# Optimization experiments

Measured on AMD Instinct MI355X. Metric: run time of the kernel, lower is better.

Reference implementation:

```python
import jax, jax.numpy as jnp
import numpy as np

N = 100000   # rows of edge_attr == number of graph nodes == number of edges (E == N required by index_add_)
B = 64       # number of graphs
IN_CH, HID, OUT_CH, FC_HID = 128, 128, 128, 256


def setup_inputs() -> dict:
    key = jax.random.key(0)
    ks = jax.random.split(key, 20)
    s = 0.05
    inp = {
        "edge_attr": jax.random.normal(ks[0], (N, 6, 120), dtype=jnp.float32),
        "edge_index": jax.random.randint(ks[1], (2, N), 0, N),
        "batch": jnp.sort(jax.random.randint(ks[2], (N,), 0, B)),
        "num_graphs": B,
        # Conv1d: in=6 -> 16 -> 32, k=5, pad=2
        "conv1_w": jax.random.normal(ks[3], (16, 6, 5), dtype=jnp.float32) * s,
        "conv1_b": jnp.zeros((16,), jnp.float32),
        "conv2_w": jax.random.normal(ks[4], (32, 16, 5), dtype=jnp.float32) * s,
        "conv2_b": jnp.zeros((32,), jnp.float32),
        # fc: 32*120 -> in_channels
        "fc_w": jax.random.normal(ks[5], (IN_CH, 32 * 120), dtype=jnp.float32) * s,
        "fc_b": jnp.zeros((IN_CH,), jnp.float32),
        # GCNConv layers (weight as [out, in], like torch Linear)
        "gcn1_w": jax.random.normal(ks[6], (HID, IN_CH), dtype=jnp.float32) * s,
        "gcn1_b": jnp.zeros((HID,), jnp.float32),
        "gcn2_w": jax.random.normal(ks[7], (OUT_CH, HID), dtype=jnp.float32) * s,
        "gcn2_b": jnp.zeros((OUT_CH,), jnp.float32),
        # MLP head
        "fc1_w": jax.random.normal(ks[8], (FC_HID, OUT_CH), dtype=jnp.float32) * s,
        "fc1_b": jnp.zeros((FC_HID,), jnp.float32),
        "fc2_w": jax.random.normal(ks[9], (OUT_CH, FC_HID), dtype=jnp.float32) * s,
        "fc2_b": jnp.zeros((OUT_CH,), jnp.float32),
    }
    return inp


def conv1d(x, w, b):
    # x: [N, C_in, L], w: [C_out, C_in, K], padding=2 (same)
    y = jax.lax.conv_general_dilated(
        x, w, window_strides=(1,), padding=[(2, 2)],
        dimension_numbers=("NCH", "OIH", "NCH"))
    return y + b[None, :, None]


def gcn_conv(x, edge_index, w, b, n_nodes):
    # PyG GCNConv: add self-loops, symmetric normalization deg^-1/2 A_hat deg^-1/2
    src, dst = edge_index[0], edge_index[1]
    loop = jnp.arange(n_nodes)
    src_f = jnp.concatenate([src, loop])
    dst_f = jnp.concatenate([dst, loop])
    deg = jax.ops.segment_sum(jnp.ones_like(src_f, dtype=x.dtype), dst_f,
                              num_segments=n_nodes)
    dinv = jnp.where(deg > 0, jax.lax.rsqrt(deg), 0.0)
    norm = dinv[src_f] * dinv[dst_f]                      # [E+N]
    h = x @ w.T                                           # [N, out]
    msg = h[src_f] * norm[:, None]                        # gather + scale
    return jax.ops.segment_sum(msg, dst_f, num_segments=n_nodes) + b


def reference(edge_attr, edge_index, batch, num_graphs,
              conv1_w, conv1_b, conv2_w, conv2_b, fc_w, fc_b,
              gcn1_w, gcn1_b, gcn2_w, gcn2_b,
              fc1_w, fc1_b, fc2_w, fc2_b):
    n = edge_attr.shape[0]
    x = jax.nn.relu(conv1d(edge_attr, conv1_w, conv1_b))   # [N,16,120]
    x = jax.nn.relu(conv1d(x, conv2_w, conv2_b))           # [N,32,120]
    x = x.reshape(n, -1)                                   # [N,3840]
    x = x @ fc_w.T + fc_b                                  # [N,in_channels]
    x = jax.nn.relu(gcn_conv(x, edge_index, gcn1_w, gcn1_b, n))
    x = gcn_conv(x, edge_index, gcn2_w, gcn2_b, n)         # [N,out_channels]
    # edge-to-batch scatter-add pooling: out[batch[row][e]] += x[e]
    row = edge_index[0]
    out = jax.ops.segment_sum(x, batch[row], num_segments=num_graphs)  # [B,out]
    x = jax.nn.relu(out @ fc1_w.T + fc1_b)
    x = x @ fc2_w.T + fc2_b
    return x
```

## Files before the change

kernel.cpp:

```cpp
#include <hip/hip_runtime.h>

typedef unsigned int u32;
typedef unsigned short u16;
typedef short short8 __attribute__((ext_vector_type(8)));
typedef float floatx4 __attribute__((ext_vector_type(4)));

static __device__ __forceinline__ u32 f2bf(float f) {
  u32 u = __float_as_uint(f);
  return (u + 0x7fffu + ((u >> 16) & 1u)) >> 16;
}
static __device__ __forceinline__ u32 cvtpk(float lo, float hi) {
  u32 r;
  asm("v_cvt_pk_bf16_f32 %0, %1, %2" : "=v"(r) : "v"(lo), "v"(hi));
  return r;
}


#define X0_ROWS 136
#define X1W_ROWS 66
#define X1W_LDA 24

__global__ __launch_bounds__(256, 2) void k_convfc(
    const float* __restrict__ ea,
    const u32* __restrict__ w1sw, const float* __restrict__ b1,
    const u32* __restrict__ w2sw, const float* __restrict__ b2,
    const u32* __restrict__ fcwsw, const float* __restrict__ fcb,
    float* __restrict__ xfc, int n, int ntiles)
{
  __shared__ __align__(16) u16 sX0[16][X0_ROWS * 8];
  __shared__ __align__(16) u16 sX1[4][X1W_ROWS * X1W_LDA];
  __shared__ __align__(16) u16 sF[32 * 64 * 8];

  const int t = threadIdx.x, lane = t & 63, wv = t >> 6;
  const int quad = lane >> 4, lr = lane & 15;

  for (int i = t; i < 16 * X0_ROWS * 4; i += 256) ((u32*)sX0)[i] = 0;

  short8 w1f[2], w2f[2][3];
#pragma unroll
  for (int kb = 0; kb < 2; ++kb) w1f[kb] = ((const short8*)w1sw)[kb * 64 + lane];
#pragma unroll
  for (int ot = 0; ot < 2; ++ot)
#pragma unroll
    for (int kb = 0; kb < 3; ++kb)
      w2f[ot][kb] = ((const short8*)w2sw)[(ot * 3 + kb) * 64 + lane];

  float b1r[4];
#pragma unroll
  for (int r = 0; r < 4; ++r) b1r[r] = b1[quad * 4 + r];
  const float bv20 = b2[lr], bv21 = b2[16 + lr];

  const int c0 = wv * 16 + lr, c1 = (wv + 4) * 16 + lr;
  const float bv0 = fcb[c0], bv1 = fcb[c1];
  const short8* bw = (const short8*)fcwsw;
  const short8* b0p = bw + ((size_t)wv * 128) * 64 + lane;
  const short8* b1p = bw + ((size_t)(wv + 4) * 128) * 64 + lane;
  const int j2base = wv * 4;

  __syncthreads();

  for (int tile = blockIdx.x; tile < ntiles; tile += gridDim.x) {
    const long node0 = (long)tile * 16;

#pragma unroll
    for (int it = 0; it < 8; ++it) {
      int idx = t + it * 256;
      int nd = idx >> 7, p = idx & 127;
      if (p < 120) {
        long gn = node0 + nd;
        float v0 = 0.f, v1 = 0.f, v2 = 0.f, v3 = 0.f, v4 = 0.f, v5 = 0.f;
        if (gn < n) {
          const float* base = ea + (size_t)gn * 720 + p;
          v0 = base[0];   v1 = base[120]; v2 = base[240];
          v3 = base[360]; v4 = base[480]; v5 = base[600];
        }
        u32 w0 = cvtpk(v0, v1), w1 = cvtpk(v2, v3), w2 = cvtpk(v4, v5);
        *(uint4*)&sX0[nd][(p + 2) * 8] = make_uint4(w0, w1, w2, 0u);
      }
    }
    __syncthreads();

    floatx4 acc0 = {bv0, bv0, bv0, bv0};
    floatx4 acc1 = {bv1, bv1, bv1, bv1};

#pragma unroll
    for (int r = 0; r < 4; ++r) {
      u16* x1 = sX1[wv];
      if (r == 0) {
        if (lane < 24) ((u32*)(x1 + 16 * X1W_LDA))[lane] = 0;
      } else if (r == 3) {
        u32* z = (u32*)(x1 + 42 * X1W_LDA);
#pragma unroll
        for (int i2 = 0; i2 < 3; ++i2) {
          int i = lane + i2 * 64;
          if (i < 132) z[i] = 0;
        }
      }
#pragma unroll 1
      for (int jj = 0; jj < 4; ++jj) {
        const int j2 = j2base + jj;
        const u16* x0n = sX0[j2];
#pragma unroll
        for (int q4 = 0; q4 < 4; ++q4) {
          const int ptp = 2 * r - 1 + q4;
          if (ptp >= 0 && ptp <= 7) {
            const int row0 = ptp * 16 + lr;
            short8 bx0 = *(const short8*)&x0n[(row0 + quad) * 8];
            short8 bx1 = *(const short8*)&x0n[(row0 + 4 + quad) * 8];
            floatx4 a1 = {b1r[0], b1r[1], b1r[2], b1r[3]};
            a1 = __builtin_amdgcn_mfma_f32_16x16x32_bf16(w1f[0], bx0, a1, 0, 0, 0);
            a1 = __builtin_amdgcn_mfma_f32_16x16x32_bf16(w1f[1], bx1, a1, 0, 0, 0);
            if (ptp < 7 || lr < 8) {
              const int lrow = row0 + 18 - 32 * r;
              u32 lo = cvtpk(fmaxf(a1[0], 0.0f), fmaxf(a1[1], 0.0f));
              u32 hi = cvtpk(fmaxf(a1[2], 0.0f), fmaxf(a1[3], 0.0f));
              *(uint2*)&x1[lrow * X1W_LDA + quad * 4] = make_uint2(lo, hi);
            }
          }
        }
        const int tq = quad >> 1, cq = (quad & 1) * 8;
#pragma unroll
        for (int ptl = 0; ptl < 2; ++ptl) {
          const int lrow0 = ptl * 16 + lr + 16;
          short8 ax0 = *(const short8*)&x1[(lrow0 + tq) * X1W_LDA + cq];
          short8 ax1 = *(const short8*)&x1[(lrow0 + 2 + tq) * X1W_LDA + cq];
          short8 ax2 = *(const short8*)&x1[(lrow0 + 4 + tq) * X1W_LDA + cq];
#pragma unroll
          for (int ot = 0; ot < 2; ++ot) {
            const float bb = ot ? bv21 : bv20;
            floatx4 a2 = {bb, bb, bb, bb};
            a2 = __builtin_amdgcn_mfma_f32_16x16x32_bf16(ax0, w2f[ot][0], a2, 0, 0, 0);
            a2 = __builtin_amdgcn_mfma_f32_16x16x32_bf16(ax1, w2f[ot][1], a2, 0, 0, 0);
            a2 = __builtin_amdgcn_mfma_f32_16x16x32_bf16(ax2, w2f[ot][2], a2, 0, 0, 0);
            u32 lo = cvtpk(fmaxf(a2[0], 0.0f), fmaxf(a2[1], 0.0f));
            u32 hi = cvtpk(fmaxf(a2[2], 0.0f), fmaxf(a2[3], 0.0f));
            const int o = ot * 16 + lr;
            const int s = (ptl * 2 + tq) * 16 + j2;
            const int G = o * 64 + (s ^ (o & 7));
            *(uint2*)&sF[G * 8 + (quad & 1) * 4] = make_uint2(lo, hi);
          }
        }
      }
      __syncthreads();

#pragma unroll 8
      for (int o = 0; o < 32; ++o) {
        short8 a = *(const short8*)&sF[(o * 64 + (lane ^ (o & 7))) * 8];
        const int ks = o * 4 + r;
        short8 bb0 = b0p[(size_t)ks * 64];
        short8 bb1 = b1p[(size_t)ks * 64];
        acc0 = __builtin_amdgcn_mfma_f32_16x16x32_bf16(a, bb0, acc0, 0, 0, 0);
        acc1 = __builtin_amdgcn_mfma_f32_16x16x32_bf16(a, bb1, acc1, 0, 0, 0);
      }
      __syncthreads();
    }

#pragma unroll
    for (int rr = 0; rr < 4; ++rr) {
      long node = node0 + quad * 4 + rr;
      if (node < n) {
        xfc[node * 128 + c0] = acc0[rr];
        xfc[node * 128 + c1] = acc1[rr];
      }
    }
  }
}

__global__ void k_prep(const float* __restrict__ fcw, const float* __restrict__ g1w,
                       const float* __restrict__ g2w, const float* __restrict__ w1,
                       const float* __restrict__ w2,
                       uint4* __restrict__ fcwsw, uint4* __restrict__ g1wsw,
                       uint4* __restrict__ g2wsw, uint4* __restrict__ w1sw,
                       uint4* __restrict__ w2sw,
                       float* __restrict__ dinv, float* __restrict__ pooled, int n)
{
  int gid = blockIdx.x * 256 + threadIdx.x;
  if (gid < 65536) {
    int e = gid, lane = e & 63, t2 = e >> 6, ks = t2 & 127, nt = t2 >> 7;
    int col = nt * 16 + (lane & 15);
    int k0 = ks * 32 + ((lane >> 4) & 3) * 8;
    u32 pk[4];
#pragma unroll
    for (int h = 0; h < 4; ++h) {
      u32 v01[2];
#pragma unroll
      for (int g = 0; g < 2; ++g) {
        int k = k0 + h * 2 + g;
        int o = k >> 7, p = k & 127;
        float v = (p < 120) ? fcw[(size_t)col * 3840 + o * 120 + p] : 0.0f;
        v01[g] = f2bf(v);
      }
      pk[h] = v01[0] | (v01[1] << 16);
    }
    fcwsw[e] = make_uint4(pk[0], pk[1], pk[2], pk[3]);
    return;
  }
  gid -= 65536;
  if (gid < 4096) {
    const float* gw = (gid < 2048) ? g1w : g2w;
    uint4* out = (gid < 2048) ? g1wsw : g2wsw;
    int e = gid & 2047, lane = e & 63;
    int col = (e >> 8) * 16 + (lane & 15);
    int k0 = ((e >> 6) & 3) * 32 + ((lane >> 4) & 3) * 8;
    u32 pk[4];
#pragma unroll
    for (int h = 0; h < 4; ++h)
      pk[h] = f2bf(gw[(size_t)col * 128 + k0 + h * 2]) |
              (f2bf(gw[(size_t)col * 128 + k0 + h * 2 + 1]) << 16);
    out[e] = make_uint4(pk[0], pk[1], pk[2], pk[3]);
    return;
  }
  gid -= 4096;
  if (gid < 128) {
    int e = gid, lane = e & 63, kb = e >> 6, cout = lane & 15;
    int k0 = kb * 32 + ((lane >> 4) & 3) * 8;
    u32 pk[4];
#pragma unroll
    for (int h = 0; h < 4; ++h) {
      u32 v01[2];
#pragma unroll
      for (int g = 0; g < 2; ++g) {
        int k = k0 + h * 2 + g, tap = k >> 3, cin = k & 7;
        float v = (tap < 5 && cin < 6) ? w1[cout * 30 + cin * 5 + tap] : 0.0f;
        v01[g] = f2bf(v);
      }
      pk[h] = v01[0] | (v01[1] << 16);
    }
    w1sw[e] = make_uint4(pk[0], pk[1], pk[2], pk[3]);
    return;
  }
  gid -= 128;
  if (gid < 384) {
    int e = gid, lane = e & 63, t2 = e >> 6;
    int kb = t2 % 3, ot = t2 / 3;
    int o = ot * 16 + (lane & 15);
    int k0 = kb * 32 + ((lane >> 4) & 3) * 8;
    u32 pk[4];
#pragma unroll
    for (int h = 0; h < 4; ++h) {
      u32 v01[2];
#pragma unroll
      for (int g = 0; g < 2; ++g) {
        int k = k0 + h * 2 + g, tap = k >> 4, c = k & 15;
        float v = (tap < 5) ? w2[o * 80 + c * 5 + tap] : 0.0f;
        v01[g] = f2bf(v);
      }
      pk[h] = v01[0] | (v01[1] << 16);
    }
    w2sw[e] = make_uint4(pk[0], pk[1], pk[2], pk[3]);
    return;
  }
  gid -= 384;
  if (gid < n) { dinv[gid] = 1.0f; return; }
  gid -= n;
  if (gid < 8192) pooled[gid] = 0.0f;
}

__global__ __launch_bounds__(256) void k_gcn_gemm(
    const float* __restrict__ X, const u32* __restrict__ wsw,
    const float* __restrict__ bias, const float* __restrict__ dinv,
    float* __restrict__ H, float* __restrict__ Out, int n, int relu)
{
  __shared__ __align__(16) u16 sA[16 * 136];
  __shared__ float sDi[16];
  const int t = threadIdx.x;
  const long node0 = (long)blockIdx.x * 16;
  {
    int nd = t >> 4, k0 = (t & 15) * 8;
    long node = node0 + nd;
    float v[8];
    if (node < n) {
      float4 f0 = *(const float4*)&X[node * 128 + k0];
      float4 f1 = *(const float4*)&X[node * 128 + k0 + 4];
      v[0]=f0.x; v[1]=f0.y; v[2]=f0.z; v[3]=f0.w; v[4]=f1.x; v[5]=f1.y; v[6]=f1.z; v[7]=f1.w;
      if (relu) {
#pragma unroll
        for (int i = 0; i < 8; ++i) v[i] = fmaxf(v[i], 0.0f);
      }
    } else {
#pragma unroll
      for (int i = 0; i < 8; ++i) v[i] = 0.0f;
    }
    u32 pk[4];
#pragma unroll
    for (int h = 0; h < 4; ++h) pk[h] = cvtpk(v[2*h], v[2*h+1]);
    *(uint4*)&sA[nd * 136 + k0] = make_uint4(pk[0], pk[1], pk[2], pk[3]);
    if (t < 16) sDi[t] = (node0 + t < n) ? dinv[node0 + t] : 0.0f;
  }
  __syncthreads();
  const int lane = t & 63, wv = t >> 6, quad = lane >> 4, lr = lane & 15;
  short8 af[4];
#pragma unroll
  for (int kb = 0; kb < 4; ++kb)
    af[kb] = *(const short8*)&sA[lr * 136 + kb * 32 + quad * 8];
#pragma unroll
  for (int h = 0; h < 2; ++h) {
    const int nt = wv + h * 4;
    const short8* bp = ((const short8*)wsw) + (nt * 4) * 64 + lane;
    floatx4 acc = {0.0f, 0.0f, 0.0f, 0.0f};
#pragma unroll
    for (int kb = 0; kb < 4; ++kb)
      acc = __builtin_amdgcn_mfma_f32_16x16x32_bf16(af[kb], bp[kb * 64], acc, 0, 0, 0);
    const int col = nt * 16 + lr;
    const float bcol = bias[col];
#pragma unroll
    for (int r = 0; r < 4; ++r) {
      long node = node0 + quad * 4 + r;
      if (node < n) {
        float hv = acc[r];
        float di = sDi[quad * 4 + r];
        H[node * 128 + col] = hv;
        Out[node * 128 + col] = bcol + di * di * hv;
      }
    }
  }
}

__global__ void k_scatter(const float* __restrict__ Hs, float* __restrict__ Out,
                          const int* __restrict__ src, const int* __restrict__ dst,
                          const float* __restrict__ dinv, int n)
{
  const int gid = blockIdx.x * blockDim.x + threadIdx.x;
  const int e = gid >> 6;
  const int lane = gid & 63;
  if (e >= n) return;
  const int s = src[e], d = dst[e];
  const float nrm = dinv[s] * dinv[d];
  const float2 v = *(const float2*)(Hs + (size_t)s * 128 + lane * 2);
  float* o = Out + (size_t)d * 128 + lane * 2;
  unsafeAtomicAdd(o, v.x * nrm);
  unsafeAtomicAdd(o + 1, v.y * nrm);
}

__global__ void k_deg(float* dinv, const int* __restrict__ dst, int n) {
  int i = blockIdx.x * 256 + threadIdx.x; if (i < n) unsafeAtomicAdd(&dinv[dst[i]], 1.0f);
}
__global__ void k_rsqrt(float* p, int n) {
  int i = blockIdx.x * 256 + threadIdx.x; if (i < n) p[i] = rsqrtf(p[i]);
}

__global__ __launch_bounds__(256) void k_pool(const float* __restrict__ X,
    const int* __restrict__ src, const int* __restrict__ batch,
    float* __restrict__ pooled, int n)
{
  __shared__ float sAcc[64 * 128];
  for (int i = threadIdx.x; i < 8192; i += 256) sAcc[i] = 0.0f;
  __syncthreads();
  const int c = threadIdx.x & 127, half = threadIdx.x >> 7;
  for (int e = blockIdx.x * 2 + half; e < n; e += gridDim.x * 2) {
    int g = batch[src[e]];
    atomicAdd(&sAcc[g * 128 + c], X[(size_t)e * 128 + c]);
  }
  __syncthreads();
  for (int i = threadIdx.x; i < 8192; i += 256) unsafeAtomicAdd(&pooled[i], sAcc[i]);
}

__global__ __launch_bounds__(256) void k_mlp(const float* __restrict__ pooled,
    const float* __restrict__ f1w, const float* __restrict__ f1b,
    const float* __restrict__ f2w, const float* __restrict__ f2b,
    float* __restrict__ out)
{
  const int g = blockIdx.x, t = threadIdx.x;
  __shared__ float sP[128];
  __shared__ float sY[256];
  if (t < 128) sP[t] = pooled[g * 128 + t];
  __syncthreads();
  {
    const float* w = f1w + (size_t)t * 128;
    float a = f1b[t];
    for (int k = 0; k < 128; k += 4) {
      float4 w4 = *(const float4*)(w + k);
      a = fmaf(w4.x, sP[k], fmaf(w4.y, sP[k+1], fmaf(w4.z, sP[k+2], fmaf(w4.w, sP[k+3], a))));
    }
    sY[t] = fmaxf(a, 0.0f);
  }
  __syncthreads();
  if (t < 128) {
    const float* w = f2w + (size_t)t * 256;
    float a = f2b[t];
    for (int k = 0; k < 256; k += 4) {
      float4 w4 = *(const float4*)(w + k);
      a = fmaf(w4.x, sY[k], fmaf(w4.y, sY[k+1], fmaf(w4.z, sY[k+2], fmaf(w4.w, sY[k+3], a))));
    }
    out[g * 128 + t] = a;
  }
}

extern "C" void kernel_launch(void* const* d_in, const int* in_sizes, int n_in,
                              void* d_out, int out_size, void* d_ws, size_t ws_size,
                              hipStream_t stream) {
  const float* ea  = (const float*)d_in[0];
  const int* eidx  = (const int*)d_in[1];
  const int* batch = (const int*)d_in[2];
  const float* w1  = (const float*)d_in[4];
  const float* b1  = (const float*)d_in[5];
  const float* w2  = (const float*)d_in[6];
  const float* b2  = (const float*)d_in[7];
  const float* fcw = (const float*)d_in[8];
  const float* fcb = (const float*)d_in[9];
  const float* g1w = (const float*)d_in[10];
  const float* g1b = (const float*)d_in[11];
  const float* g2w = (const float*)d_in[12];
  const float* g2b = (const float*)d_in[13];
  const float* f1w = (const float*)d_in[14];
  const float* f1b = (const float*)d_in[15];
  const float* f2w = (const float*)d_in[16];
  const float* f2b = (const float*)d_in[17];

  const int n = in_sizes[0] / 720;
  const int* src = eidx;
  const int* dst = eidx + n;

  float* A      = (float*)d_ws;
  float* B      = A + (size_t)n * 128;
  float* C      = B + (size_t)n * 128;
  float* dinv   = C + (size_t)n * 128;
  float* pooled = dinv + n;
  u32*   fcwsw  = (u32*)(pooled + 64 * 128);
  u32*   g1wsw  = fcwsw + 65536 * 4;
  u32*   g2wsw  = g1wsw + 2048 * 4;
  u32*   w1sw   = g2wsw + 2048 * 4;
  u32*   w2sw   = w1sw + 128 * 4;

  const int nb_n = (n + 255) / 256;
  const int ntiles = (n + 15) / 16;
  const int prep_total = 65536 + 2048 + 2048 + 128 + 384 + n + 8192;
  k_prep<<<(prep_total + 255) / 256, 256, 0, stream>>>(
      fcw, g1w, g2w, w1, w2, (uint4*)fcwsw, (uint4*)g1wsw, (uint4*)g2wsw,
      (uint4*)w1sw, (uint4*)w2sw, dinv, pooled, n);
  k_deg<<<nb_n, 256, 0, stream>>>(dinv, dst, n);
  k_rsqrt<<<nb_n, 256, 0, stream>>>(dinv, n);

  k_convfc<<<512, 256, 0, stream>>>(ea, w1sw, b1, w2sw, b2, fcwsw, fcb, A, n, ntiles);

  k_gcn_gemm<<<(n + 15) / 16, 256, 0, stream>>>(A, g1wsw, g1b, dinv, B, C, n, 0);
  k_scatter<<<((size_t)n * 64 + 255) / 256, 256, 0, stream>>>(B, C, src, dst, dinv, n);

  k_gcn_gemm<<<(n + 15) / 16, 256, 0, stream>>>(C, g2wsw, g2b, dinv, A, B, n, 1);
  k_scatter<<<((size_t)n * 64 + 255) / 256, 256, 0, stream>>>(A, B, src, dst, dinv, n);

  k_pool<<<256, 256, 0, stream>>>(B, src, batch, pooled, n);
  k_mlp<<<64, 256, 0, stream>>>(pooled, f1w, f1b, f2w, f2b, (float*)d_out);
}
```

Before: 1.144 ms.

## Software-pipeline next tile's input loads and prefetch fc weights behind conv compute

After: 1.337 ms. 1.17x slower.

```diff
diff --git a/kernel.cpp b/kernel.cpp
--- a/kernel.cpp
+++ b/kernel.cpp
@@ -57,11 +57,70 @@
   const short8* b1p = bw + ((size_t)(wv + 4) * 128) * 64 + lane;
   const int j2base = wv * 4;
 
-  __syncthreads();
-
-  for (int tile = blockIdx.x; tile < ntiles; tile += gridDim.x) {
+  auto conv_round = [&](int r) {
+    u16* x1 = sX1[wv];
+    if (r == 0) {
+      if (lane < 24) ((u32*)(x1 + 16 * X1W_LDA))[lane] = 0;
+    } else if (r == 3) {
+      u32* z = (u32*)(x1 + 42 * X1W_LDA);
+#pragma unroll
+      for (int i2 = 0; i2 < 3; ++i2) {
+        int i = lane + i2 * 64;
+        if (i < 132) z[i] = 0;
+      }
+    }
+    const int tq = quad >> 1, cq = (quad & 1) * 8;
+#pragma unroll
+    for (int jj = 0; jj < 4; ++jj) {
+      const int j2 = j2base + jj;
+      const u16* x0n = sX0[j2];
+#pragma unroll
+      for (int q4 = 0; q4 < 4; ++q4) {
+        const int ptp = 2 * r - 1 + q4;
+        if (ptp >= 0 && ptp <= 7) {
+          const int row0 = ptp * 16 + lr;
+          short8 bx0 = *(const short8*)&x0n[(row0 + quad) * 8];
+          short8 bx1 = *(const short8*)&x0n[(row0 + 4 + quad) * 8];
+          floatx4 a1 = {b1r[0], b1r[1], b1r[2], b1r[3]};
+          a1 = __builtin_amdgcn_mfma_f32_16x16x32_bf16(w1f[0], bx0, a1, 0, 0, 0);
+          a1 = __builtin_amdgcn_mfma_f32_16x16x32_bf16(w1f[1], bx1, a1, 0, 0, 0);
+          if (ptp < 7 || lr < 8) {
+            const int lrow = row0 + 18 - 32 * r;
+            u32 lo = cvtpk(fmaxf(a1[0], 0.0f), fmaxf(a1[1], 0.0f));
+            u32 hi = cvtpk(fmaxf(a1[2], 0.0f), fmaxf(a1[3], 0.0f));
+            *(uint2*)&x1[lrow * X1W_LDA + quad * 4] = make_uint2(lo, hi);
+          }
+        }
+      }
+#pragma unroll
+      for (int ptl = 0; ptl < 2; ++ptl) {
+        const int lrow0 = ptl * 16 + lr + 16;
+        short8 ax0 = *(const short8*)&x1[(lrow0 + tq) * X1W_LDA + cq];
+        short8 ax1 = *(const short8*)&x1[(lrow0 + 2 + tq) * X1W_LDA + cq];
+        short8 ax2 = *(const short8*)&x1[(lrow0 + 4 + tq) * X1W_LDA + cq];
+#pragma unroll
+        for (int ot = 0; ot < 2; ++ot) {
+          const float bb = ot ? bv21 : bv20;
+          floatx4 a2 = {bb, bb, bb, bb};
+          a2 = __builtin_amdgcn_mfma_f32_16x16x32_bf16(ax0, w2f[ot][0], a2, 0, 0, 0);
+          a2 = __builtin_amdgcn_mfma_f32_16x16x32_bf16(ax1, w2f[ot][1], a2, 0, 0, 0);
+          a2 = __builtin_amdgcn_mfma_f32_16x16x32_bf16(ax2, w2f[ot][2], a2, 0, 0, 0);
+          u32 lo = cvtpk(fmaxf(a2[0], 0.0f), fmaxf(a2[1], 0.0f));
+          u32 hi = cvtpk(fmaxf(a2[2], 0.0f), fmaxf(a2[3], 0.0f));
+          const int o = ot * 16 + lr;
+          const int s = (ptl * 2 + tq) * 16 + j2;
+          const int G = o * 64 + (s ^ (o & 7));
+          *(uint2*)&sF[G * 8 + (quad & 1) * 4] = make_uint2(lo, hi);
+        }
+      }
+    }
+  };
+
+  __syncthreads();
+
+  int tile = blockIdx.x;
+  if (tile < ntiles) {
     const long node0 = (long)tile * 16;
-
 #pragma unroll
     for (int it = 0; it < 8; ++it) {
       int idx = t + it * 256;
@@ -78,73 +137,33 @@
         *(uint4*)&sX0[nd][(p + 2) * 8] = make_uint4(w0, w1, w2, 0u);
       }
     }
-    __syncthreads();
-
+  }
+  __syncthreads();
+
+  for (; tile < ntiles; tile += gridDim.x) {
+    const long node0 = (long)tile * 16;
     floatx4 acc0 = {bv0, bv0, bv0, bv0};
     floatx4 acc1 = {bv1, bv1, bv1, bv1};
 
 #pragma unroll
-    for (int r = 0; r < 4; ++r) {
-      u16* x1 = sX1[wv];
-      if (r == 0) {
-        if (lane < 24) ((u32*)(x1 + 16 * X1W_LDA))[lane] = 0;
-      } else if (r == 3) {
-        u32* z = (u32*)(x1 + 42 * X1W_LDA);
-#pragma unroll
-        for (int i2 = 0; i2 < 3; ++i2) {
-          int i = lane + i2 * 64;
-          if (i < 132) z[i] = 0;
-        }
-      }
-#pragma unroll 1
-      for (int jj = 0; jj < 4; ++jj) {
-        const int j2 = j2base + jj;
-        const u16* x0n = sX0[j2];
-#pragma unroll
-        for (int q4 = 0; q4 < 4; ++q4) {
-          const int ptp = 2 * r - 1 + q4;
-          if (ptp >= 0 && ptp <= 7) {
-            const int row0 = ptp * 16 + lr;
-            short8 bx0 = *(const short8*)&x0n[(row0 + quad) * 8];
-            short8 bx1 = *(const short8*)&x0n[(row0 + 4 + quad) * 8];
-            floatx4 a1 = {b1r[0], b1r[1], b1r[2], b1r[3]};
-            a1 = __builtin_amdgcn_mfma_f32_16x16x32_bf16(w1f[0], bx0, a1, 0, 0, 0);
-            a1 = __builtin_amdgcn_mfma_f32_16x16x32_bf16(w1f[1], bx1, a1, 0, 0, 0);
-            if (ptp < 7 || lr < 8) {
-              const int lrow = row0 + 18 - 32 * r;
-              u32 lo = cvtpk(fmaxf(a1[0], 0.0f), fmaxf(a1[1], 0.0f));
-              u32 hi = cvtpk(fmaxf(a1[2], 0.0f), fmaxf(a1[3], 0.0f));
-              *(uint2*)&x1[lrow * X1W_LDA + quad * 4] = make_uint2(lo, hi);
-            }
-          }
-        }
-        const int tq = quad >> 1, cq = (quad & 1) * 8;
-#pragma unroll
-        for (int ptl = 0; ptl < 2; ++ptl) {
-          const int lrow0 = ptl * 16 + lr + 16;
-          short8 ax0 = *(const short8*)&x1[(lrow0 + tq) * X1W_LDA + cq];
-          short8 ax1 = *(const short8*)&x1[(lrow0 + 2 + tq) * X1W_LDA + cq];
-          short8 ax2 = *(const short8*)&x1[(lrow0 + 4 + tq) * X1W_LDA + cq];
-#pragma unroll
-          for (int ot = 0; ot < 2; ++ot) {
-            const float bb = ot ? bv21 : bv20;
-            floatx4 a2 = {bb, bb, bb, bb};
-            a2 = __builtin_amdgcn_mfma_f32_16x16x32_bf16(ax0, w2f[ot][0], a2, 0, 0, 0);
-            a2 = __builtin_amdgcn_mfma_f32_16x16x32_bf16(ax1, w2f[ot][1], a2, 0, 0, 0);
-            a2 = __builtin_amdgcn_mfma_f32_16x16x32_bf16(ax2, w2f[ot][2], a2, 0, 0, 0);
-            u32 lo = cvtpk(fmaxf(a2[0], 0.0f), fmaxf(a2[1], 0.0f));
-            u32 hi = cvtpk(fmaxf(a2[2], 0.0f), fmaxf(a2[3], 0.0f));
-            const int o = ot * 16 + lr;
-            const int s = (ptl * 2 + tq) * 16 + j2;
-            const int G = o * 64 + (s ^ (o & 7));
-            *(uint2*)&sF[G * 8 + (quad & 1) * 4] = make_uint2(lo, hi);
-          }
-        }
-      }
+    for (int r = 0; r < 3; ++r) {
+      short8 pb0[8], pb1[8];
+#pragma unroll
+      for (int o = 0; o < 8; ++o) {
+        const int ks = o * 4 + r;
+        pb0[o] = b0p[(size_t)ks * 64];
+        pb1[o] = b1p[(size_t)ks * 64];
+      }
+      conv_round(r);
       __syncthreads();
-
+#pragma unroll
+      for (int o = 0; o < 8; ++o) {
+        short8 a = *(const short8*)&sF[(o * 64 + (lane ^ (o & 7))) * 8];
+        acc0 = __builtin_amdgcn_mfma_f32_16x16x32_bf16(a, pb0[o], acc0, 0, 0, 0);
+        acc1 = __builtin_amdgcn_mfma_f32_16x16x32_bf16(a, pb1[o], acc1, 0, 0, 0);
+      }
 #pragma unroll 8
-      for (int o = 0; o < 32; ++o) {
+      for (int o = 8; o < 32; ++o) {
         short8 a = *(const short8*)&sF[(o * 64 + (lane ^ (o & 7))) * 8];
         const int ks = o * 4 + r;
         short8 bb0 = b0p[(size_t)ks * 64];
@@ -155,6 +174,48 @@
       __syncthreads();
     }
 
+    const long ntnode0 = ((long)tile + gridDim.x) * 16;
+    float ev[8][6];
+#pragma unroll
+    for (int it = 0; it < 8; ++it) {
+      int idx = t + it * 256;
+      int nd = idx >> 7, p = idx & 127;
+#pragma unroll
+      for (int c6 = 0; c6 < 6; ++c6) ev[it][c6] = 0.0f;
+      if (p < 120) {
+        long gn = ntnode0 + nd;
+        if (gn < n) {
+          const float* base = ea + (size_t)gn * 720 + p;
+          ev[it][0] = base[0];   ev[it][1] = base[120]; ev[it][2] = base[240];
+          ev[it][3] = base[360]; ev[it][4] = base[480]; ev[it][5] = base[600];
+        }
+      }
+    }
+    conv_round(3);
+    __syncthreads();
+
+#pragma unroll
+    for (int it = 0; it < 8; ++it) {
+      int idx = t + it * 256;
+      int nd = idx >> 7, p = idx & 127;
+      if (p < 120) {
+        u32 w0 = cvtpk(ev[it][0], ev[it][1]);
+        u32 w1 = cvtpk(ev[it][2], ev[it][3]);
+        u32 w2 = cvtpk(ev[it][4], ev[it][5]);
+        *(uint4*)&sX0[nd][(p + 2) * 8] = make_uint4(w0, w1, w2, 0u);
+      }
+    }
+
+#pragma unroll 8
+    for (int o = 0; o < 32; ++o) {
+      short8 a = *(const short8*)&sF[(o * 64 + (lane ^ (o & 7))) * 8];
+      const int ks = o * 4 + 3;
+      short8 bb0 = b0p[(size_t)ks * 64];
+      short8 bb1 = b1p[(size_t)ks * 64];
+      acc0 = __builtin_amdgcn_mfma_f32_16x16x32_bf16(a, bb0, acc0, 0, 0, 0);
+      acc1 = __builtin_amdgcn_mfma_f32_16x16x32_bf16(a, bb1, acc1, 0, 0, 0);
+    }
+
 #pragma unroll
     for (int rr = 0; rr < 4; ++rr) {
       long node = node0 + quad * 4 + rr;
@@ -163,6 +224,7 @@
         xfc[node * 128 + c1] = acc1[rr];
       }
     }
+    __syncthreads();
   }
 }
 
```

## Build CSR by destination, gather-based aggregation, fuse GCN1 GEMM into conv-fc kernel

Applied to the files above, without the earlier changes.

Result: faster. 1.074 ms (-6.2%).

```diff
diff --git a/kernel.cpp b/kernel.cpp
--- a/kernel.cpp
+++ b/kernel.cpp
@@ -25,11 +25,14 @@
     const u32* __restrict__ w1sw, const float* __restrict__ b1,
     const u32* __restrict__ w2sw, const float* __restrict__ b2,
     const u32* __restrict__ fcwsw, const float* __restrict__ fcb,
-    float* __restrict__ xfc, int n, int ntiles)
+    const u32* __restrict__ g1wsw, const float* __restrict__ g1b,
+    const float* __restrict__ dinv,
+    float* __restrict__ H1, float* __restrict__ OutC, int n, int ntiles)
 {
   __shared__ __align__(16) u16 sX0[16][X0_ROWS * 8];
   __shared__ __align__(16) u16 sX1[4][X1W_ROWS * X1W_LDA];
   __shared__ __align__(16) u16 sF[32 * 64 * 8];
+  __shared__ float sDi[16];
 
   const int t = threadIdx.x, lane = t & 63, wv = t >> 6;
   const int quad = lane >> 4, lr = lane & 15;
@@ -52,9 +55,12 @@
 
   const int c0 = wv * 16 + lr, c1 = (wv + 4) * 16 + lr;
   const float bv0 = fcb[c0], bv1 = fcb[c1];
+  const float gb0 = g1b[c0], gb1 = g1b[c1];
   const short8* bw = (const short8*)fcwsw;
   const short8* b0p = bw + ((size_t)wv * 128) * 64 + lane;
   const short8* b1p = bw + ((size_t)(wv + 4) * 128) * 64 + lane;
+  const short8* gp0 = ((const short8*)g1wsw) + (wv * 4) * 64 + lane;
+  const short8* gp1 = ((const short8*)g1wsw) + ((wv + 4) * 4) * 64 + lane;
   const int j2base = wv * 4;
 
   __syncthreads();
@@ -143,6 +149,7 @@
       }
       __syncthreads();
 
+      __builtin_amdgcn_s_setprio(1);
 #pragma unroll 8
       for (int o = 0; o < 32; ++o) {
         short8 a = *(const short8*)&sF[(o * 64 + (lane ^ (o & 7))) * 8];
@@ -152,15 +159,40 @@
         acc0 = __builtin_amdgcn_mfma_f32_16x16x32_bf16(a, bb0, acc0, 0, 0, 0);
         acc1 = __builtin_amdgcn_mfma_f32_16x16x32_bf16(a, bb1, acc1, 0, 0, 0);
       }
+      __builtin_amdgcn_s_setprio(0);
       __syncthreads();
     }
 
-#pragma unroll
-    for (int rr = 0; rr < 4; ++rr) {
-      long node = node0 + quad * 4 + rr;
-      if (node < n) {
-        xfc[node * 128 + c0] = acc0[rr];
-        xfc[node * 128 + c1] = acc1[rr];
+    {
+      u16* sT = sF;
+      if (t < 16) sDi[t] = (node0 + t < n) ? dinv[node0 + t] : 0.0f;
+#pragma unroll
+      for (int rr = 0; rr < 4; ++rr) {
+        const int nd = quad * 4 + rr;
+        sT[nd * 136 + c0] = (u16)cvtpk(acc0[rr], acc0[rr]);
+        sT[nd * 136 + c1] = (u16)cvtpk(acc1[rr], acc1[rr]);
+      }
+      __syncthreads();
+      short8 af[4];
+#pragma unroll
+      for (int kb = 0; kb < 4; ++kb)
+        af[kb] = *(const short8*)&sT[lr * 136 + kb * 32 + quad * 8];
+      floatx4 h0 = {0.f, 0.f, 0.f, 0.f}, h1 = {0.f, 0.f, 0.f, 0.f};
+#pragma unroll
+      for (int kb = 0; kb < 4; ++kb) {
+        h0 = __builtin_amdgcn_mfma_f32_16x16x32_bf16(af[kb], gp0[kb * 64], h0, 0, 0, 0);
+        h1 = __builtin_amdgcn_mfma_f32_16x16x32_bf16(af[kb], gp1[kb * 64], h1, 0, 0, 0);
+      }
+#pragma unroll
+      for (int rr = 0; rr < 4; ++rr) {
+        long node = node0 + quad * 4 + rr;
+        if (node < n) {
+          float di = sDi[quad * 4 + rr];
+          H1[node * 128 + c0] = h0[rr];
+          H1[node * 128 + c1] = h1[rr];
+          OutC[node * 128 + c0] = gb0 + di * di * h0[rr];
+          OutC[node * 128 + c1] = gb1 + di * di * h1[rr];
+        }
       }
     }
   }
@@ -172,7 +204,8 @@
                        uint4* __restrict__ fcwsw, uint4* __restrict__ g1wsw,
                        uint4* __restrict__ g2wsw, uint4* __restrict__ w1sw,
                        uint4* __restrict__ w2sw,
-                       float* __restrict__ dinv, float* __restrict__ pooled, int n)
+                       float* __restrict__ dinv, float* __restrict__ pooled,
+                       int* __restrict__ degi, int n)
 {
   int gid = blockIdx.x * 256 + threadIdx.x;
   if (gid < 65536) {
@@ -253,7 +286,77 @@
   gid -= 384;
   if (gid < n) { dinv[gid] = 1.0f; return; }
   gid -= n;
-  if (gid < 8192) pooled[gid] = 0.0f;
+  if (gid < 8192) { pooled[gid] = 0.0f; return; }
+  gid -= 8192;
+  if (gid < n) degi[gid] = 0;
+}
+
+__global__ void k_deg(float* dinv, int* __restrict__ degi,
+                      const int* __restrict__ dst, int n) {
+  int i = blockIdx.x * 256 + threadIdx.x;
+  if (i < n) {
+    int d = dst[i];
+    unsafeAtomicAdd(&dinv[d], 1.0f);
+    atomicAdd(&degi[d], 1);
+  }
+}
+__global__ void k_rsqrt(float* p, int n) {
+  int i = blockIdx.x * 256 + threadIdx.x; if (i < n) p[i] = rsqrtf(p[i]);
+}
+
+__global__ void k_scan1(const int* __restrict__ degi, int* __restrict__ bsum, int n) {
+  __shared__ int s[256];
+  int b = blockIdx.x, t = threadIdx.x, i = b * 256 + t;
+  s[t] = (i < n) ? degi[i] : 0;
+  __syncthreads();
+  for (int o = 128; o > 0; o >>= 1) {
+    if (t < o) s[t] += s[t + o];
+    __syncthreads();
+  }
+  if (t == 0) bsum[b] = s[0];
+}
+__global__ void k_scan2(const int* __restrict__ bsum, int* __restrict__ boff,
+                        int* __restrict__ off, int nb, int n) {
+  __shared__ int s[512];
+  int t = threadIdx.x;
+  int v = (t < nb) ? bsum[t] : 0;
+  s[t] = v;
+  __syncthreads();
+  for (int o = 1; o < 512; o <<= 1) {
+    int x = (t >= o) ? s[t - o] : 0;
+    __syncthreads();
+    s[t] += x;
+    __syncthreads();
+  }
+  if (t < nb) boff[t] = s[t] - v;
+  if (t == 511) off[n] = s[511];
+}
+__global__ void k_scan3(const int* __restrict__ degi, const int* __restrict__ boff,
+                        int* __restrict__ off, int* __restrict__ fillptr, int n) {
+  __shared__ int s[256];
+  int b = blockIdx.x, t = threadIdx.x, i = b * 256 + t;
+  int v = (i < n) ? degi[i] : 0;
+  s[t] = v;
+  __syncthreads();
+  for (int o = 1; o < 256; o <<= 1) {
+    int x = (t >= o) ? s[t - o] : 0;
+    __syncthreads();
+    s[t] += x;
+    __syncthreads();
+  }
+  if (i < n) {
+    int e = boff[b] + s[t] - v;
+    off[i] = e;
+    fillptr[i] = e;
+  }
+}
+__global__ void k_fill(const int* __restrict__ src, const int* __restrict__ dst,
+                       int* __restrict__ fillptr, int* __restrict__ csr, int n) {
+  int e = blockIdx.x * 256 + threadIdx.x;
+  if (e < n) {
+    int slot = atomicAdd(&fillptr[dst[e]], 1);
+    csr[slot] = src[e];
+  }
 }
 
 __global__ __launch_bounds__(256) void k_gcn_gemm(
@@ -316,27 +419,27 @@
   }
 }
 
-__global__ void k_scatter(const float* __restrict__ Hs, float* __restrict__ Out,
-                          const int* __restrict__ src, const int* __restrict__ dst,
-                          const float* __restrict__ dinv, int n)
+__global__ __launch_bounds__(256) void k_gather(
+    const float* __restrict__ H, float* __restrict__ Out,
+    const int* __restrict__ off, const int* __restrict__ csr,
+    const float* __restrict__ dinv, int n)
 {
   const int gid = blockIdx.x * blockDim.x + threadIdx.x;
-  const int e = gid >> 6;
+  const int d = gid >> 6;
   const int lane = gid & 63;
-  if (e >= n) return;
-  const int s = src[e], d = dst[e];
-  const float nrm = dinv[s] * dinv[d];
-  const float2 v = *(const float2*)(Hs + (size_t)s * 128 + lane * 2);
-  float* o = Out + (size_t)d * 128 + lane * 2;
-  unsafeAtomicAdd(o, v.x * nrm);
-  unsafeAtomicAdd(o + 1, v.y * nrm);
-}
-
-__global__ void k_deg(float* dinv, const int* __restrict__ dst, int n) {
-  int i = blockIdx.x * 256 + threadIdx.x; if (i < n) unsafeAtomicAdd(&dinv[dst[i]], 1.0f);
-}
-__global__ void k_rsqrt(float* p, int n) {
-  int i = blockIdx.x * 256 + threadIdx.x; if (i < n) p[i] = rsqrtf(p[i]);
+  if (d >= n) return;
+  const int j0 = off[d], j1 = off[d + 1];
+  if (j0 == j1) return;
+  const float dd = dinv[d];
+  float2 acc = *(const float2*)(Out + (size_t)d * 128 + lane * 2);
+  for (int j = j0; j < j1; ++j) {
+    const int s = csr[j];
+    const float nrm = dinv[s] * dd;
+    const float2 v = *(const float2*)(H + (size_t)s * 128 + lane * 2);
+    acc.x = fmaf(v.x, nrm, acc.x);
+    acc.y = fmaf(v.y, nrm, acc.y);
+  }
+  *(float2*)(Out + (size_t)d * 128 + lane * 2) = acc;
 }
 
 __global__ __launch_bounds__(256) void k_pool(const float* __restrict__ X,
@@ -421,23 +524,33 @@
   u32*   g2wsw  = g1wsw + 2048 * 4;
   u32*   w1sw   = g2wsw + 2048 * 4;
   u32*   w2sw   = w1sw + 128 * 4;
+  int*   off    = (int*)(w2sw + 384 * 4);
+  int*   csr    = off + (n + 1);
+  int*   degi    = (int*)A;
+  int*   fillptr = degi + n;
+  int*   bsum    = fillptr + n;
+  int*   boff    = bsum + 512;
 
   const int nb_n = (n + 255) / 256;
   const int ntiles = (n + 15) / 16;
-  const int prep_total = 65536 + 2048 + 2048 + 128 + 384 + n + 8192;
+  const int prep_total = 65536 + 2048 + 2048 + 128 + 384 + n + 8192 + n;
   k_prep<<<(prep_total + 255) / 256, 256, 0, stream>>>(
       fcw, g1w, g2w, w1, w2, (uint4*)fcwsw, (uint4*)g1wsw, (uint4*)g2wsw,
-      (uint4*)w1sw, (uint4*)w2sw, dinv, pooled, n);
-  k_deg<<<nb_n, 256, 0, stream>>>(dinv, dst, n);
+      (uint4*)w1sw, (uint4*)w2sw, dinv, pooled, degi, n);
+  k_deg<<<nb_n, 256, 0, stream>>>(dinv, degi, dst, n);
   k_rsqrt<<<nb_n, 256, 0, stream>>>(dinv, n);
-
-  k_convfc<<<512, 256, 0, stream>>>(ea, w1sw, b1, w2sw, b2, fcwsw, fcb, A, n, ntiles);
-
-  k_gcn_gemm<<<(n + 15) / 16, 256, 0, stream>>>(A, g1wsw, g1b, dinv, B, C, n, 0);
-  k_scatter<<<((size_t)n * 64 + 255) / 256, 256, 0, stream>>>(B, C, src, dst, dinv, n);
+  k_scan1<<<nb_n, 256, 0, stream>>>(degi, bsum, n);
+  k_scan2<<<1, 512, 0, stream>>>(bsum, boff, off, nb_n, n);
+  k_scan3<<<nb_n, 256, 0, stream>>>(degi, boff, off, fillptr, n);
+  k_fill<<<nb_n, 256, 0, stream>>>(src, dst, fillptr, csr, n);
+
+  k_convfc<<<512, 256, 0, stream>>>(ea, w1sw, b1, w2sw, b2, fcwsw, fcb,
+                                    g1wsw, g1b, dinv, B, C, n, ntiles);
+
+  k_gather<<<(int)(((size_t)n * 64 + 255) / 256), 256, 0, stream>>>(B, C, off, csr, dinv, n);
 
   k_gcn_gemm<<<(n + 15) / 16, 256, 0, stream>>>(C, g2wsw, g2b, dinv, A, B, n, 1);
-  k_scatter<<<((size_t)n * 64 + 255) / 256, 256, 0, stream>>>(A, B, src, dst, dinv, n);
+  k_gather<<<(int)(((size_t)n * 64 + 255) / 256), 256, 0, stream>>>(A, B, off, csr, dinv, n);
 
   k_pool<<<256, 256, 0, stream>>>(B, src, batch, pooled, n);
   k_mlp<<<64, 256, 0, stream>>>(pooled, f1w, f1b, f2w, f2b, (float*)d_out);
```
